# Optimization experiments

Hardware: AMD Instinct MI355X
Metric: run time of the kernel (lower is better)

Reference implementation:

```python
import jax, jax.numpy as jnp
import numpy as np

DIM = 1024
NUM_HEADS = 8  # only used for the scale; heads are never actually split
SCALE = float((DIM // NUM_HEADS) ** 0.5)


def _attn(x, wq, wk, wv):
    # Single-head full-dim attention, faithful to the source (no head split).
    Q = x @ wq.T  # [B,S,D]
    K = x @ wk.T
    V = x @ wv.T
    scores = jnp.einsum('bqd,bkd->bqk', Q, K) / SCALE  # [B,S,S]
    attn = jax.nn.softmax(scores, axis=-1)
    return jnp.einsum('bqk,bkd->bqd', attn, V)


def setup_inputs() -> dict:
    key = jax.random.key(0)
    ks = jax.random.split(key, 9)
    B, S, D = 4, 2048, DIM
    w = lambda k: jax.random.normal(k, (D, D), dtype=jnp.float32) * 0.02
    return {
        'x': jax.random.normal(ks[0], (B, S, D), dtype=jnp.float32),
        'wq1': w(ks[1]), 'wk1': w(ks[2]), 'wv1': w(ks[3]),
        'fc1_w': w(ks[4]),
        'wq2': w(ks[5]), 'wk2': w(ks[6]), 'wv2': w(ks[7]),
        'fc2_w': w(ks[8]),
    }


def reference(x, wq1, wk1, wv1, fc1_w, wq2, wk2, wv2, fc2_w):
    h = _attn(x, wq1, wk1, wv1)
    h = jax.nn.silu(h)
    h = h @ fc1_w.T
    h = _attn(h, wq2, wk2, wv2)
    h = jax.nn.silu(h)
    h = h @ fc2_w.T
    return jax.nn.softmax(h, axis=-1)
```

## Files before the change

kernel.cpp:

```cpp
#include <hip/hip_runtime.h>
#include <math.h>


typedef __attribute__((ext_vector_type(8))) int i32x8;
typedef __attribute__((ext_vector_type(4))) int i32x4;
typedef __attribute__((ext_vector_type(4))) float f32x4;
typedef unsigned char u8;
typedef unsigned int u32;

#define EPI_F32 0
#define EPI_F8 1
#define EPI_QKV 2
#define EPI_EXP 3
#define EPI_PV 4

__device__ __forceinline__ void gload_lds16(const void* g, void* l) {
    __builtin_amdgcn_global_load_lds(
        (const __attribute__((address_space(1))) void*)g,
        (__attribute__((address_space(3))) void*)l, 16, 0, 0);
}

__device__ __forceinline__ u8 cvt_f8(float v) {
    return (u8)(__builtin_amdgcn_cvt_pk_fp8_f32(v, v, 0, false) & 0xFF);
}

template <int EPI>
__global__ __launch_bounds__(256) void gemm_fp8(
    const u8* __restrict__ A, const u8* __restrict__ B,
    void* __restrict__ C0, void* __restrict__ C1, void* __restrict__ C2,
    int K, int ldA, int ldB, int ldC,
    long long bsA, long long bsB, long long bsC, float alpha, float beta)
{
    __shared__ u8 sA[128 * 128];
    __shared__ u8 sB[128 * 128];

    const int tid = threadIdx.x;
    const int wave = tid >> 6, lane = tid & 63;
    const int wm = wave >> 1, wn = wave & 1;
    const int m0 = blockIdx.y * 128, n0 = blockIdx.x * 128;
    const long long z = blockIdx.z;

    const u8* pA = A + z * bsA;
    const u8* pB = B + z * bsB;

    int blkid[4], rs_[4], cs16[4];
#pragma unroll
    for (int i = 0; i < 4; i++) {
        blkid[i] = wave * 256 + i * 64 + lane;
        rs_[i] = blkid[i] >> 3;
        cs16[i] = ((blkid[i] & 7) ^ (rs_[i] & 7)) * 16;
    }

    f32x4 acc[4][4] = {};
    const int fr = lane & 15, fc2 = (lane >> 4) * 2;

    for (int k0 = 0; k0 < K; k0 += 128) {
#pragma unroll
        for (int i = 0; i < 4; i++) {
            gload_lds16(pA + (long long)(m0 + rs_[i]) * ldA + k0 + cs16[i],
                        sA + blkid[i] * 16);
            gload_lds16(pB + (long long)(n0 + rs_[i]) * ldB + k0 + cs16[i],
                        sB + blkid[i] * 16);
        }
        __syncthreads();

        i32x8 a[4], b[4];
#pragma unroll
        for (int i = 0; i < 4; i++) {
            const int row = wm * 64 + i * 16 + fr;
            const int sw = row & 7;
            i32x4 lo = *(const i32x4*)(sA + row * 128 + ((fc2 + 0) ^ sw) * 16);
            i32x4 hi = *(const i32x4*)(sA + row * 128 + ((fc2 + 1) ^ sw) * 16);
            a[i] = __builtin_shufflevector(lo, hi, 0, 1, 2, 3, 4, 5, 6, 7);
        }
#pragma unroll
        for (int j = 0; j < 4; j++) {
            const int row = wn * 64 + j * 16 + fr;
            const int sw = row & 7;
            i32x4 lo = *(const i32x4*)(sB + row * 128 + ((fc2 + 0) ^ sw) * 16);
            i32x4 hi = *(const i32x4*)(sB + row * 128 + ((fc2 + 1) ^ sw) * 16);
            b[j] = __builtin_shufflevector(lo, hi, 0, 1, 2, 3, 4, 5, 6, 7);
        }
#pragma unroll
        for (int i = 0; i < 4; i++)
#pragma unroll
            for (int j = 0; j < 4; j++)
                acc[i][j] = __builtin_amdgcn_mfma_scale_f32_16x16x128_f8f6f4(
                    a[i], b[j], acc[i][j], 0 , 0 ,
                    0, 0x7F7F7F7F, 0, 0x7F7F7F7F);
        __syncthreads();
    }

    const int col = lane & 15;
    const int rbase = (lane >> 4) * 4;

    if (EPI == EPI_EXP) {
        u8* P = (u8*)C0 + z * bsC;
        float* rsum = (float*)C1 + z * 2048;
#pragma unroll
        for (int i = 0; i < 4; i++) {
            const int mloc = m0 + wm * 64 + i * 16 + rbase;
            float rowp[4] = {0.f, 0.f, 0.f, 0.f};
#pragma unroll
            for (int j = 0; j < 4; j++) {
                const int nloc = n0 + wn * 64 + j * 16 + col;
#pragma unroll
                for (int r = 0; r < 4; r++) {
                    float e = __expf(acc[i][j][r] * alpha);
                    rowp[r] += e;
                    P[(long long)(mloc + r) * ldC + nloc] = cvt_f8(e * 0.0625f);
                }
            }
#pragma unroll
            for (int r = 0; r < 4; r++) {
                float t = rowp[r];
                t += __shfl_xor(t, 1);
                t += __shfl_xor(t, 2);
                t += __shfl_xor(t, 4);
                t += __shfl_xor(t, 8);
                if ((lane & 15) == 0) atomicAdd(&rsum[mloc + r], t);
            }
        }
        return;
    }

#pragma unroll
    for (int i = 0; i < 4; i++) {
        const int mloc = m0 + wm * 64 + i * 16 + rbase;
        float inv[4];
        if (EPI == EPI_PV) {
            const float* rsum = (const float*)C1 + z * 2048;
#pragma unroll
            for (int r = 0; r < 4; r++) inv[r] = alpha / rsum[mloc + r];
        }
#pragma unroll
        for (int j = 0; j < 4; j++) {
            const int nloc = n0 + wn * 64 + j * 16 + col;
            if (EPI == EPI_F32) {
                float* C = (float*)C0 + z * bsC;
#pragma unroll
                for (int r = 0; r < 4; r++)
                    C[(long long)(mloc + r) * ldC + nloc] = acc[i][j][r] * alpha;
            } else if (EPI == EPI_F8) {
                u8* C = (u8*)C0 + z * bsC;
#pragma unroll
                for (int r = 0; r < 4; r++)
                    C[(long long)(mloc + r) * ldC + nloc] =
                        cvt_f8(acc[i][j][r] * alpha);
            } else if (EPI == EPI_PV) {
                u8* C = (u8*)C0 + z * bsC;
#pragma unroll
                for (int r = 0; r < 4; r++) {
                    float v = acc[i][j][r] * inv[r];
                    v = v / (1.f + __expf(-v));
                    C[(long long)(mloc + r) * ldC + nloc] = cvt_f8(v * beta);
                }
            } else {
                const int seg = nloc >> 10;
                const int nn = nloc & 1023;
                float v[4];
#pragma unroll
                for (int r = 0; r < 4; r++) v[r] = acc[i][j][r] * alpha;
                if (seg == 2) {
                    const int bb = mloc >> 11, mm = mloc & 2047;
                    int p01 = __builtin_amdgcn_cvt_pk_fp8_f32(v[0], v[1], 0, false);
                    int p23 = __builtin_amdgcn_cvt_pk_fp8_f32(v[2], v[3], 0, false);
                    u32 pk = (u32)(p01 & 0xFFFF) | ((u32)p23 << 16);
                    *(u32*)((u8*)C2 + (long long)bb * (1024LL * 2048) +
                            (long long)nn * 2048 + mm) = pk;
                } else {
                    u8* C = seg ? (u8*)C1 : (u8*)C0;
#pragma unroll
                    for (int r = 0; r < 4; r++)
                        C[(long long)(mloc + r) * 1024 + nn] = cvt_f8(v[r]);
                }
            }
        }
    }
}

__global__ __launch_bounds__(256) void convert_fp8(
    const float* __restrict__ in, u8* __restrict__ o, long long n, float scale)
{
    long long i = ((long long)blockIdx.x * 256 + threadIdx.x) * 4;
    if (i >= n) return;
    float4 v = *(const float4*)(in + i);
    int p01 = __builtin_amdgcn_cvt_pk_fp8_f32(v.x * scale, v.y * scale, 0, false);
    int p23 = __builtin_amdgcn_cvt_pk_fp8_f32(v.z * scale, v.w * scale, 0, false);
    *(u32*)(o + i) = (u32)(p01 & 0xFFFF) | ((u32)p23 << 16);
}

__global__ __launch_bounds__(256) void convert_w8(
    const float* w0, const float* w1, const float* w2, const float* w3,
    const float* w4, const float* w5, const float* w6, const float* w7,
    u8* __restrict__ o)
{
    const float* ws[8] = {w0, w1, w2, w3, w4, w5, w6, w7};
    const float* src = ws[blockIdx.y];
    long long i = ((long long)blockIdx.x * 256 + threadIdx.x) * 4;
    float4 v = *(const float4*)(src + i);
    int p01 = __builtin_amdgcn_cvt_pk_fp8_f32(v.x * 256.f, v.y * 256.f, 0, false);
    int p23 = __builtin_amdgcn_cvt_pk_fp8_f32(v.z * 256.f, v.w * 256.f, 0, false);
    *(u32*)(o + (long long)blockIdx.y * 1024 * 1024 + i) =
        (u32)(p01 & 0xFFFF) | ((u32)p23 << 16);
}

__global__ __launch_bounds__(256) void softmax_1024(
    const float* __restrict__ in, float* __restrict__ out)
{
    const float* p = in + (long long)blockIdx.x * 1024;
    float* o = out + (long long)blockIdx.x * 1024;
    const int tid = threadIdx.x;
    const int lane = tid & 63, wv = tid >> 6;
    __shared__ float redm[4], reds[4];

    float4 v = *(const float4*)(p + tid * 4);
    float vals[4] = {v.x, v.y, v.z, v.w};

    float m = -INFINITY;
#pragma unroll
    for (int i = 0; i < 4; i++) m = fmaxf(m, vals[i]);
#pragma unroll
    for (int off = 32; off; off >>= 1) m = fmaxf(m, __shfl_xor(m, off));
    if (lane == 0) redm[wv] = m;
    __syncthreads();
    m = fmaxf(fmaxf(redm[0], redm[1]), fmaxf(redm[2], redm[3]));

    float s = 0.f;
#pragma unroll
    for (int i = 0; i < 4; i++) {
        vals[i] = __expf(vals[i] - m);
        s += vals[i];
    }
#pragma unroll
    for (int off = 32; off; off >>= 1) s += __shfl_xor(s, off);
    if (lane == 0) reds[wv] = s;
    __syncthreads();
    s = reds[0] + reds[1] + reds[2] + reds[3];
    const float inv = 1.0f / s;
    float4 ov;
    ov.x = vals[0] * inv; ov.y = vals[1] * inv;
    ov.z = vals[2] * inv; ov.w = vals[3] * inv;
    *(float4*)(o + tid * 4) = ov;
}

extern "C" void kernel_launch(void* const* d_in, const int* in_sizes, int n_in,
                              void* d_out, int out_size, void* d_ws, size_t ws_size,
                              hipStream_t stream)
{
    const float* x = (const float*)d_in[0];
    float* out = (float*)d_out;

    constexpr int Bt = 4, S = 2048, D = 1024;
    constexpr int M = Bt * S;
    const long long MD = (long long)M * D;
    const long long DD = (long long)D * D;
    const long long SD = (long long)S * D;
    const long long SS = (long long)S * S;

    u8* Af = (u8*)d_ws;
    u8* Wf = Af + MD;
    u8* Qf = Wf + 8 * DD;
    u8* Kf = Qf + MD;
    u8* VT = Kf + MD;
    u8* Pf = VT + MD;
    u8* Hs = Pf + (long long)Bt * SS;
    float* SC = (float*)(Hs + MD);
    float* rsum = SC + MD;

    const dim3 blk(256);

    const float SOFT = 0.08838834764831845f;
    const float a_qkv[2] = {8.f / 2048.f, 1024.f / 65536.f};
    const float a_qk[2]  = {SOFT / 64.f, SOFT / 1048576.f};
    const float a_pv[2]  = {2.0f, 1.f / 64.f};
    const float b_pv[2]  = {256.f, 65536.f};
    const float a_fc[2]  = {256.f / 65536.f, 1.f / 16777216.f};

    convert_fp8<<<dim3((int)(MD / 1024)), blk, 0, stream>>>(x, Af, MD, 8.f);
    convert_w8<<<dim3((int)(DD / 1024), 8), blk, 0, stream>>>(
        (const float*)d_in[1], (const float*)d_in[2], (const float*)d_in[3],
        (const float*)d_in[4], (const float*)d_in[5], (const float*)d_in[6],
        (const float*)d_in[7], (const float*)d_in[8], Wf);

    const dim3 gqkv(3 * D / 128, M / 128, 1);
    const dim3 gw(D / 128, M / 128, 1);
    const dim3 gqk(S / 128, S / 128, Bt);
    const dim3 gpv(D / 128, S / 128, Bt);

    for (int layer = 0; layer < 2; layer++) {
        const u8* wqkv = Wf + (long long)(layer * 4) * DD;
        const u8* fc   = Wf + (long long)(layer * 4 + 3) * DD;

        gemm_fp8<EPI_QKV><<<gqkv, blk, 0, stream>>>(
            Af, wqkv, Qf, Kf, VT, D, D, D, D, 0, 0, 0, a_qkv[layer], 0.f);
        hipMemsetAsync(rsum, 0, (size_t)M * sizeof(float), stream);
        gemm_fp8<EPI_EXP><<<gqk, blk, 0, stream>>>(
            Qf, Kf, Pf, rsum, nullptr, D, D, D, S, SD, SD, SS,
            a_qk[layer], 0.f);
        gemm_fp8<EPI_PV><<<gpv, blk, 0, stream>>>(
            Pf, VT, Hs, rsum, nullptr, S, S, S, D, SS, (long long)D * S, SD,
            a_pv[layer], b_pv[layer]);
        if (layer == 0) {
            gemm_fp8<EPI_F8><<<gw, blk, 0, stream>>>(
                Hs, fc, Af, nullptr, nullptr, D, D, D, D, 0, 0, 0,
                a_fc[0], 0.f);
        } else {
            gemm_fp8<EPI_F32><<<gw, blk, 0, stream>>>(
                Hs, fc, SC, nullptr, nullptr, D, D, D, D, 0, 0, 0,
                a_fc[1], 0.f);
        }
    }

    softmax_1024<<<dim3(M), blk, 0, stream>>>(SC, out);
}
```

Measured before the change: 347.8 us.

## Switch FP8 GEMM to 32x32x64 MFMA and fold rsum zeroing into weight conversion

The FP8 GEMM now uses the 32x32x64 scaled MFMA with a 2x2 accumulator tile per wave instead of 4x4 tiles of 16x16x128. The K step is split into two halves, and every epilogue is remapped to the 32x32 output layout, including the row-sum shuffle reduction, the transposed V store and the per-row inverse loads. This is meant to cut LDS fragment reads and MFMA issue count for the same work. Separately, the per-layer hipMemsetAsync of the row-sum buffer is dropped. Both layers' sums are instead zeroed inside the weight-conversion kernel, using two separate buffers, which saves two launches but needs workspace room for the second buffer.

```diff
diff --git a/kernel.cpp b/kernel.cpp
--- a/kernel.cpp
+++ b/kernel.cpp
@@ -4,7 +4,7 @@
 
 typedef __attribute__((ext_vector_type(8))) int i32x8;
 typedef __attribute__((ext_vector_type(4))) int i32x4;
-typedef __attribute__((ext_vector_type(4))) float f32x4;
+typedef __attribute__((ext_vector_type(16))) float f32x16;
 typedef unsigned char u8;
 typedef unsigned int u32;
 
@@ -51,8 +51,10 @@
         cs16[i] = ((blkid[i] & 7) ^ (rs_[i] & 7)) * 16;
     }
 
-    f32x4 acc[4][4] = {};
-    const int fr = lane & 15, fc2 = (lane >> 4) * 2;
+    f32x16 acc[2][2] = {};
+    const int l31 = lane & 31;
+    const int lh = lane >> 5;
+    const int half4 = lh * 4;
 
     for (int k0 = 0; k0 < K; k0 += 128) {
 #pragma unroll
@@ -64,115 +66,138 @@
         }
         __syncthreads();
 
-        i32x8 a[4], b[4];
-#pragma unroll
-        for (int i = 0; i < 4; i++) {
-            const int row = wm * 64 + i * 16 + fr;
-            const int sw = row & 7;
-            i32x4 lo = *(const i32x4*)(sA + row * 128 + ((fc2 + 0) ^ sw) * 16);
-            i32x4 hi = *(const i32x4*)(sA + row * 128 + ((fc2 + 1) ^ sw) * 16);
-            a[i] = __builtin_shufflevector(lo, hi, 0, 1, 2, 3, 4, 5, 6, 7);
-        }
-#pragma unroll
-        for (int j = 0; j < 4; j++) {
-            const int row = wn * 64 + j * 16 + fr;
-            const int sw = row & 7;
-            i32x4 lo = *(const i32x4*)(sB + row * 128 + ((fc2 + 0) ^ sw) * 16);
-            i32x4 hi = *(const i32x4*)(sB + row * 128 + ((fc2 + 1) ^ sw) * 16);
-            b[j] = __builtin_shufflevector(lo, hi, 0, 1, 2, 3, 4, 5, 6, 7);
-        }
-#pragma unroll
-        for (int i = 0; i < 4; i++)
-#pragma unroll
-            for (int j = 0; j < 4; j++)
-                acc[i][j] = __builtin_amdgcn_mfma_scale_f32_16x16x128_f8f6f4(
-                    a[i], b[j], acc[i][j], 0 , 0 ,
-                    0, 0x7F7F7F7F, 0, 0x7F7F7F7F);
+#pragma unroll
+        for (int h = 0; h < 2; h++) {
+            const int c0 = h * 4 + lh * 2;
+            i32x8 a[2], b[2];
+#pragma unroll
+            for (int i = 0; i < 2; i++) {
+                const int row = wm * 64 + i * 32 + l31;
+                const int sw = row & 7;
+                i32x4 lo = *(const i32x4*)(sA + row * 128 + ((c0 + 0) ^ sw) * 16);
+                i32x4 hi = *(const i32x4*)(sA + row * 128 + ((c0 + 1) ^ sw) * 16);
+                a[i] = __builtin_shufflevector(lo, hi, 0, 1, 2, 3, 4, 5, 6, 7);
+            }
+#pragma unroll
+            for (int j = 0; j < 2; j++) {
+                const int row = wn * 64 + j * 32 + l31;
+                const int sw = row & 7;
+                i32x4 lo = *(const i32x4*)(sB + row * 128 + ((c0 + 0) ^ sw) * 16);
+                i32x4 hi = *(const i32x4*)(sB + row * 128 + ((c0 + 1) ^ sw) * 16);
+                b[j] = __builtin_shufflevector(lo, hi, 0, 1, 2, 3, 4, 5, 6, 7);
+            }
+#pragma unroll
+            for (int i = 0; i < 2; i++)
+#pragma unroll
+                for (int j = 0; j < 2; j++)
+                    acc[i][j] = __builtin_amdgcn_mfma_scale_f32_32x32x64_f8f6f4(
+                        a[i], b[j], acc[i][j], 0 , 0 ,
+                        0, 0x7F7F7F7F, 0, 0x7F7F7F7F);
+        }
         __syncthreads();
     }
 
-    const int col = lane & 15;
-    const int rbase = (lane >> 4) * 4;
+    const int col = l31;
 
     if (EPI == EPI_EXP) {
         u8* P = (u8*)C0 + z * bsC;
         float* rsum = (float*)C1 + z * 2048;
 #pragma unroll
-        for (int i = 0; i < 4; i++) {
-            const int mloc = m0 + wm * 64 + i * 16 + rbase;
-            float rowp[4] = {0.f, 0.f, 0.f, 0.f};
-#pragma unroll
-            for (int j = 0; j < 4; j++) {
-                const int nloc = n0 + wn * 64 + j * 16 + col;
-#pragma unroll
-                for (int r = 0; r < 4; r++) {
-                    float e = __expf(acc[i][j][r] * alpha);
-                    rowp[r] += e;
-                    P[(long long)(mloc + r) * ldC + nloc] = cvt_f8(e * 0.0625f);
-                }
-            }
-#pragma unroll
-            for (int r = 0; r < 4; r++) {
-                float t = rowp[r];
+        for (int i = 0; i < 2; i++) {
+            const int mbase = m0 + wm * 64 + i * 32;
+            float rowp[16];
+#pragma unroll
+            for (int g = 0; g < 16; g++) rowp[g] = 0.f;
+#pragma unroll
+            for (int j = 0; j < 2; j++) {
+                const int nloc = n0 + wn * 64 + j * 32 + col;
+#pragma unroll
+                for (int g = 0; g < 16; g++) {
+                    const int mloc = mbase + (g & 3) + 8 * (g >> 2) + half4;
+                    float e = __expf(acc[i][j][g] * alpha);
+                    rowp[g] += e;
+                    P[(long long)mloc * ldC + nloc] = cvt_f8(e * 0.0625f);
+                }
+            }
+#pragma unroll
+            for (int g = 0; g < 16; g++) {
+                float t = rowp[g];
                 t += __shfl_xor(t, 1);
                 t += __shfl_xor(t, 2);
                 t += __shfl_xor(t, 4);
                 t += __shfl_xor(t, 8);
-                if ((lane & 15) == 0) atomicAdd(&rsum[mloc + r], t);
+                t += __shfl_xor(t, 16);
+                if (col == 0) {
+                    const int mloc = mbase + (g & 3) + 8 * (g >> 2) + half4;
+                    atomicAdd(&rsum[mloc], t);
+                }
             }
         }
         return;
     }
 
 #pragma unroll
-    for (int i = 0; i < 4; i++) {
-        const int mloc = m0 + wm * 64 + i * 16 + rbase;
-        float inv[4];
+    for (int i = 0; i < 2; i++) {
+        const int mbase = m0 + wm * 64 + i * 32;
+        float inv[16];
         if (EPI == EPI_PV) {
             const float* rsum = (const float*)C1 + z * 2048;
 #pragma unroll
-            for (int r = 0; r < 4; r++) inv[r] = alpha / rsum[mloc + r];
-        }
-#pragma unroll
-        for (int j = 0; j < 4; j++) {
-            const int nloc = n0 + wn * 64 + j * 16 + col;
+            for (int g = 0; g < 16; g++)
+                inv[g] = alpha / rsum[mbase + (g & 3) + 8 * (g >> 2) + half4];
+        }
+#pragma unroll
+        for (int j = 0; j < 2; j++) {
+            const int nloc = n0 + wn * 64 + j * 32 + col;
             if (EPI == EPI_F32) {
                 float* C = (float*)C0 + z * bsC;
 #pragma unroll
-                for (int r = 0; r < 4; r++)
-                    C[(long long)(mloc + r) * ldC + nloc] = acc[i][j][r] * alpha;
+                for (int g = 0; g < 16; g++) {
+                    const int mloc = mbase + (g & 3) + 8 * (g >> 2) + half4;
+                    C[(long long)mloc * ldC + nloc] = acc[i][j][g] * alpha;
+                }
             } else if (EPI == EPI_F8) {
                 u8* C = (u8*)C0 + z * bsC;
 #pragma unroll
-                for (int r = 0; r < 4; r++)
-                    C[(long long)(mloc + r) * ldC + nloc] =
-                        cvt_f8(acc[i][j][r] * alpha);
+                for (int g = 0; g < 16; g++) {
+                    const int mloc = mbase + (g & 3) + 8 * (g >> 2) + half4;
+                    C[(long long)mloc * ldC + nloc] = cvt_f8(acc[i][j][g] * alpha);
+                }
             } else if (EPI == EPI_PV) {
                 u8* C = (u8*)C0 + z * bsC;
 #pragma unroll
-                for (int r = 0; r < 4; r++) {
-                    float v = acc[i][j][r] * inv[r];
+                for (int g = 0; g < 16; g++) {
+                    const int mloc = mbase + (g & 3) + 8 * (g >> 2) + half4;
+                    float v = acc[i][j][g] * inv[g];
                     v = v / (1.f + __expf(-v));
-                    C[(long long)(mloc + r) * ldC + nloc] = cvt_f8(v * beta);
+                    C[(long long)mloc * ldC + nloc] = cvt_f8(v * beta);
                 }
             } else {
                 const int seg = nloc >> 10;
                 const int nn = nloc & 1023;
-                float v[4];
-#pragma unroll
-                for (int r = 0; r < 4; r++) v[r] = acc[i][j][r] * alpha;
                 if (seg == 2) {
-                    const int bb = mloc >> 11, mm = mloc & 2047;
-                    int p01 = __builtin_amdgcn_cvt_pk_fp8_f32(v[0], v[1], 0, false);
-                    int p23 = __builtin_amdgcn_cvt_pk_fp8_f32(v[2], v[3], 0, false);
-                    u32 pk = (u32)(p01 & 0xFFFF) | ((u32)p23 << 16);
-                    *(u32*)((u8*)C2 + (long long)bb * (1024LL * 2048) +
-                            (long long)nn * 2048 + mm) = pk;
+#pragma unroll
+                    for (int g = 0; g < 4; g++) {
+                        const int mloc = mbase + 8 * g + half4;
+                        const int bb = mloc >> 11, mm = mloc & 2047;
+                        float v0 = acc[i][j][4 * g + 0] * alpha;
+                        float v1 = acc[i][j][4 * g + 1] * alpha;
+                        float v2 = acc[i][j][4 * g + 2] * alpha;
+                        float v3 = acc[i][j][4 * g + 3] * alpha;
+                        int p01 = __builtin_amdgcn_cvt_pk_fp8_f32(v0, v1, 0, false);
+                        int p23 = __builtin_amdgcn_cvt_pk_fp8_f32(v2, v3, 0, false);
+                        u32 pk = (u32)(p01 & 0xFFFF) | ((u32)p23 << 16);
+                        *(u32*)((u8*)C2 + (long long)bb * (1024LL * 2048) +
+                                (long long)nn * 2048 + mm) = pk;
+                    }
                 } else {
                     u8* C = seg ? (u8*)C1 : (u8*)C0;
 #pragma unroll
-                    for (int r = 0; r < 4; r++)
-                        C[(long long)(mloc + r) * 1024 + nn] = cvt_f8(v[r]);
+                    for (int g = 0; g < 16; g++) {
+                        const int mloc = mbase + (g & 3) + 8 * (g >> 2) + half4;
+                        C[(long long)mloc * 1024 + nn] =
+                            cvt_f8(acc[i][j][g] * alpha);
+                    }
                 }
             }
         }
@@ -193,8 +218,12 @@
 __global__ __launch_bounds__(256) void convert_w8(
     const float* w0, const float* w1, const float* w2, const float* w3,
     const float* w4, const float* w5, const float* w6, const float* w7,
-    u8* __restrict__ o)
-{
+    u8* __restrict__ o, float* __restrict__ rz)
+{
+    if (blockIdx.y == 0 && blockIdx.x < 16) {
+        float4 zero = {0.f, 0.f, 0.f, 0.f};
+        *(float4*)(rz + ((long long)blockIdx.x * 256 + threadIdx.x) * 4) = zero;
+    }
     const float* ws[8] = {w0, w1, w2, w3, w4, w5, w6, w7};
     const float* src = ws[blockIdx.y];
     long long i = ((long long)blockIdx.x * 256 + threadIdx.x) * 4;
@@ -266,7 +295,8 @@
     u8* Pf = VT + MD;
     u8* Hs = Pf + (long long)Bt * SS;
     float* SC = (float*)(Hs + MD);
-    float* rsum = SC + MD;
+    float* rsum0 = SC + MD;
+    float* rsum1 = rsum0 + M;
 
     const dim3 blk(256);
 
@@ -281,7 +311,7 @@
     convert_w8<<<dim3((int)(DD / 1024), 8), blk, 0, stream>>>(
         (const float*)d_in[1], (const float*)d_in[2], (const float*)d_in[3],
         (const float*)d_in[4], (const float*)d_in[5], (const float*)d_in[6],
-        (const float*)d_in[7], (const float*)d_in[8], Wf);
+        (const float*)d_in[7], (const float*)d_in[8], Wf, rsum0);
 
     const dim3 gqkv(3 * D / 128, M / 128, 1);
     const dim3 gw(D / 128, M / 128, 1);
@@ -291,10 +321,10 @@
     for (int layer = 0; layer < 2; layer++) {
         const u8* wqkv = Wf + (long long)(layer * 4) * DD;
         const u8* fc   = Wf + (long long)(layer * 4 + 3) * DD;
+        float* rsum    = layer ? rsum1 : rsum0;
 
         gemm_fp8<EPI_QKV><<<gqkv, blk, 0, stream>>>(
             Af, wqkv, Qf, Kf, VT, D, D, D, D, 0, 0, 0, a_qkv[layer], 0.f);
-        hipMemsetAsync(rsum, 0, (size_t)M * sizeof(float), stream);
         gemm_fp8<EPI_EXP><<<gqk, blk, 0, stream>>>(
             Qf, Kf, Pf, rsum, nullptr, D, D, D, S, SD, SD, SS,
             a_qk[layer], 0.f);
```

Result: slower. 373.4 us (+7.3%).

## Fuse final exp and row-sum into fc2 GEMM epilogue, merge conversions and memsets

Applied to the files above, without the earlier changes.

The last GEMM's epilogue now writes exp(logits) and atomically accumulates per-row sums, so the final softmax becomes a single normalize pass without max or sum reductions. The two input-conversion kernels are merged into one launch that also zeroes three row-sum buffers, which removes the per-layer memsets. This drops the max subtraction, so it relies on the logits staying small enough not to overflow, and it adds atomic traffic to the fc2 epilogue.

```diff
diff --git a/kernel.cpp b/kernel.cpp
--- a/kernel.cpp
+++ b/kernel.cpp
@@ -8,11 +8,11 @@
 typedef unsigned char u8;
 typedef unsigned int u32;
 
-#define EPI_F32 0
 #define EPI_F8 1
 #define EPI_QKV 2
 #define EPI_EXP 3
 #define EPI_PV 4
+#define EPI_EXPF32 5
 
 __device__ __forceinline__ void gload_lds16(const void* g, void* l) {
     __builtin_amdgcn_global_load_lds(
@@ -94,12 +94,13 @@
     const int col = lane & 15;
     const int rbase = (lane >> 4) * 4;
 
-    if (EPI == EPI_EXP) {
+    if (EPI == EPI_EXP || EPI == EPI_EXPF32) {
         u8* P = (u8*)C0 + z * bsC;
-        float* rsum = (float*)C1 + z * 2048;
+        float* Cw = (float*)C0 + z * bsC;
+        float* rsum = (EPI == EPI_EXP) ? ((float*)C1 + z * 2048) : (float*)C1;
 #pragma unroll
         for (int i = 0; i < 4; i++) {
-            const int mloc = m0 + wm * 64 + i * 16 + rbase;
+            const int mloc0 = m0 + wm * 64 + i * 16 + rbase;
             float rowp[4] = {0.f, 0.f, 0.f, 0.f};
 #pragma unroll
             for (int j = 0; j < 4; j++) {
@@ -108,7 +109,11 @@
                 for (int r = 0; r < 4; r++) {
                     float e = __expf(acc[i][j][r] * alpha);
                     rowp[r] += e;
-                    P[(long long)(mloc + r) * ldC + nloc] = cvt_f8(e * 0.0625f);
+                    if (EPI == EPI_EXP)
+                        P[(long long)(mloc0 + r) * ldC + nloc] =
+                            cvt_f8(e * 0.0625f);
+                    else
+                        Cw[(long long)(mloc0 + r) * ldC + nloc] = e;
                 }
             }
 #pragma unroll
@@ -118,7 +123,7 @@
                 t += __shfl_xor(t, 2);
                 t += __shfl_xor(t, 4);
                 t += __shfl_xor(t, 8);
-                if ((lane & 15) == 0) atomicAdd(&rsum[mloc + r], t);
+                if ((lane & 15) == 0) atomicAdd(&rsum[mloc0 + r], t);
             }
         }
         return;
@@ -126,26 +131,21 @@
 
 #pragma unroll
     for (int i = 0; i < 4; i++) {
-        const int mloc = m0 + wm * 64 + i * 16 + rbase;
+        const int mloc0 = m0 + wm * 64 + i * 16 + rbase;
         float inv[4];
         if (EPI == EPI_PV) {
             const float* rsum = (const float*)C1 + z * 2048;
 #pragma unroll
-            for (int r = 0; r < 4; r++) inv[r] = alpha / rsum[mloc + r];
+            for (int r = 0; r < 4; r++) inv[r] = alpha / rsum[mloc0 + r];
         }
 #pragma unroll
         for (int j = 0; j < 4; j++) {
             const int nloc = n0 + wn * 64 + j * 16 + col;
-            if (EPI == EPI_F32) {
-                float* C = (float*)C0 + z * bsC;
+            if (EPI == EPI_F8) {
+                u8* C = (u8*)C0 + z * bsC;
 #pragma unroll
                 for (int r = 0; r < 4; r++)
-                    C[(long long)(mloc + r) * ldC + nloc] = acc[i][j][r] * alpha;
-            } else if (EPI == EPI_F8) {
-                u8* C = (u8*)C0 + z * bsC;
-#pragma unroll
-                for (int r = 0; r < 4; r++)
-                    C[(long long)(mloc + r) * ldC + nloc] =
+                    C[(long long)(mloc0 + r) * ldC + nloc] =
                         cvt_f8(acc[i][j][r] * alpha);
             } else if (EPI == EPI_PV) {
                 u8* C = (u8*)C0 + z * bsC;
@@ -153,7 +153,7 @@
                 for (int r = 0; r < 4; r++) {
                     float v = acc[i][j][r] * inv[r];
                     v = v / (1.f + __expf(-v));
-                    C[(long long)(mloc + r) * ldC + nloc] = cvt_f8(v * beta);
+                    C[(long long)(mloc0 + r) * ldC + nloc] = cvt_f8(v * beta);
                 }
             } else {
                 const int seg = nloc >> 10;
@@ -162,7 +162,7 @@
 #pragma unroll
                 for (int r = 0; r < 4; r++) v[r] = acc[i][j][r] * alpha;
                 if (seg == 2) {
-                    const int bb = mloc >> 11, mm = mloc & 2047;
+                    const int bb = mloc0 >> 11, mm = mloc0 & 2047;
                     int p01 = __builtin_amdgcn_cvt_pk_fp8_f32(v[0], v[1], 0, false);
                     int p23 = __builtin_amdgcn_cvt_pk_fp8_f32(v[2], v[3], 0, false);
                     u32 pk = (u32)(p01 & 0xFFFF) | ((u32)p23 << 16);
@@ -172,83 +172,62 @@
                     u8* C = seg ? (u8*)C1 : (u8*)C0;
 #pragma unroll
                     for (int r = 0; r < 4; r++)
-                        C[(long long)(mloc + r) * 1024 + nn] = cvt_f8(v[r]);
+                        C[(long long)(mloc0 + r) * 1024 + nn] = cvt_f8(v[r]);
                 }
             }
         }
     }
 }
 
-__global__ __launch_bounds__(256) void convert_fp8(
-    const float* __restrict__ in, u8* __restrict__ o, long long n, float scale)
-{
-    long long i = ((long long)blockIdx.x * 256 + threadIdx.x) * 4;
-    if (i >= n) return;
-    float4 v = *(const float4*)(in + i);
+__global__ __launch_bounds__(256) void convert_all(
+    const float* x, const float* w0, const float* w1, const float* w2,
+    const float* w3, const float* w4, const float* w5, const float* w6,
+    const float* w7, u8* __restrict__ ax, u8* __restrict__ wf,
+    float* __restrict__ rz)
+{
+    const int bid = blockIdx.x;
+    if (bid < 24) {
+        float4 zero = {0.f, 0.f, 0.f, 0.f};
+        *(float4*)(rz + ((long long)bid * 256 + threadIdx.x) * 4) = zero;
+    }
+    const float* src;
+    u8* dst;
+    float scale;
+    long long i;
+    if (bid < 8192) {
+        src = x; dst = ax; scale = 8.f;
+        i = ((long long)bid * 256 + threadIdx.x) * 4;
+    } else {
+        const float* ws[8] = {w0, w1, w2, w3, w4, w5, w6, w7};
+        const int wi = (bid - 8192) >> 10;
+        src = ws[wi]; scale = 256.f;
+        dst = wf + (long long)wi * 1024 * 1024;
+        i = (((long long)(bid - 8192) & 1023) * 256 + threadIdx.x) * 4;
+    }
+    float4 v = *(const float4*)(src + i);
     int p01 = __builtin_amdgcn_cvt_pk_fp8_f32(v.x * scale, v.y * scale, 0, false);
     int p23 = __builtin_amdgcn_cvt_pk_fp8_f32(v.z * scale, v.w * scale, 0, false);
-    *(u32*)(o + i) = (u32)(p01 & 0xFFFF) | ((u32)p23 << 16);
-}
-
-__global__ __launch_bounds__(256) void convert_w8(
-    const float* w0, const float* w1, const float* w2, const float* w3,
-    const float* w4, const float* w5, const float* w6, const float* w7,
-    u8* __restrict__ o)
-{
-    const float* ws[8] = {w0, w1, w2, w3, w4, w5, w6, w7};
-    const float* src = ws[blockIdx.y];
-    long long i = ((long long)blockIdx.x * 256 + threadIdx.x) * 4;
-    float4 v = *(const float4*)(src + i);
-    int p01 = __builtin_amdgcn_cvt_pk_fp8_f32(v.x * 256.f, v.y * 256.f, 0, false);
-    int p23 = __builtin_amdgcn_cvt_pk_fp8_f32(v.z * 256.f, v.w * 256.f, 0, false);
-    *(u32*)(o + (long long)blockIdx.y * 1024 * 1024 + i) =
-        (u32)(p01 & 0xFFFF) | ((u32)p23 << 16);
-}
-
-__global__ __launch_bounds__(256) void softmax_1024(
-    const float* __restrict__ in, float* __restrict__ out)
-{
-    const float* p = in + (long long)blockIdx.x * 1024;
-    float* o = out + (long long)blockIdx.x * 1024;
-    const int tid = threadIdx.x;
-    const int lane = tid & 63, wv = tid >> 6;
-    __shared__ float redm[4], reds[4];
-
-    float4 v = *(const float4*)(p + tid * 4);
-    float vals[4] = {v.x, v.y, v.z, v.w};
-
-    float m = -INFINITY;
-#pragma unroll
-    for (int i = 0; i < 4; i++) m = fmaxf(m, vals[i]);
-#pragma unroll
-    for (int off = 32; off; off >>= 1) m = fmaxf(m, __shfl_xor(m, off));
-    if (lane == 0) redm[wv] = m;
-    __syncthreads();
-    m = fmaxf(fmaxf(redm[0], redm[1]), fmaxf(redm[2], redm[3]));
-
-    float s = 0.f;
-#pragma unroll
-    for (int i = 0; i < 4; i++) {
-        vals[i] = __expf(vals[i] - m);
-        s += vals[i];
-    }
-#pragma unroll
-    for (int off = 32; off; off >>= 1) s += __shfl_xor(s, off);
-    if (lane == 0) reds[wv] = s;
-    __syncthreads();
-    s = reds[0] + reds[1] + reds[2] + reds[3];
-    const float inv = 1.0f / s;
+    *(u32*)(dst + i) = (u32)(p01 & 0xFFFF) | ((u32)p23 << 16);
+}
+
+__global__ __launch_bounds__(256) void normalize_1024(
+    const float* __restrict__ e, const float* __restrict__ rsum,
+    float* __restrict__ out)
+{
+    const long long row = blockIdx.x;
+    const float inv = 1.0f / rsum[row];
+    const float* p = e + row * 1024;
+    float* o = out + row * 1024;
+    float4 v = *(const float4*)(p + threadIdx.x * 4);
     float4 ov;
-    ov.x = vals[0] * inv; ov.y = vals[1] * inv;
-    ov.z = vals[2] * inv; ov.w = vals[3] * inv;
-    *(float4*)(o + tid * 4) = ov;
+    ov.x = v.x * inv; ov.y = v.y * inv; ov.z = v.z * inv; ov.w = v.w * inv;
+    *(float4*)(o + threadIdx.x * 4) = ov;
 }
 
 extern "C" void kernel_launch(void* const* d_in, const int* in_sizes, int n_in,
                               void* d_out, int out_size, void* d_ws, size_t ws_size,
                               hipStream_t stream)
 {
-    const float* x = (const float*)d_in[0];
     float* out = (float*)d_out;
 
     constexpr int Bt = 4, S = 2048, D = 1024;
@@ -266,7 +245,9 @@
     u8* Pf = VT + MD;
     u8* Hs = Pf + (long long)Bt * SS;
     float* SC = (float*)(Hs + MD);
-    float* rsum = SC + MD;
+    float* rsum0 = SC + MD;
+    float* rsum1 = rsum0 + M;
+    float* rsum2 = rsum1 + M;
 
     const dim3 blk(256);
 
@@ -277,11 +258,11 @@
     const float b_pv[2]  = {256.f, 65536.f};
     const float a_fc[2]  = {256.f / 65536.f, 1.f / 16777216.f};
 
-    convert_fp8<<<dim3((int)(MD / 1024)), blk, 0, stream>>>(x, Af, MD, 8.f);
-    convert_w8<<<dim3((int)(DD / 1024), 8), blk, 0, stream>>>(
-        (const float*)d_in[1], (const float*)d_in[2], (const float*)d_in[3],
-        (const float*)d_in[4], (const float*)d_in[5], (const float*)d_in[6],
-        (const float*)d_in[7], (const float*)d_in[8], Wf);
+    convert_all<<<dim3(16384), blk, 0, stream>>>(
+        (const float*)d_in[0], (const float*)d_in[1], (const float*)d_in[2],
+        (const float*)d_in[3], (const float*)d_in[4], (const float*)d_in[5],
+        (const float*)d_in[6], (const float*)d_in[7], (const float*)d_in[8],
+        Af, Wf, rsum0);
 
     const dim3 gqkv(3 * D / 128, M / 128, 1);
     const dim3 gw(D / 128, M / 128, 1);
@@ -291,10 +272,10 @@
     for (int layer = 0; layer < 2; layer++) {
         const u8* wqkv = Wf + (long long)(layer * 4) * DD;
         const u8* fc   = Wf + (long long)(layer * 4 + 3) * DD;
+        float* rsum    = layer ? rsum1 : rsum0;
 
         gemm_fp8<EPI_QKV><<<gqkv, blk, 0, stream>>>(
             Af, wqkv, Qf, Kf, VT, D, D, D, D, 0, 0, 0, a_qkv[layer], 0.f);
-        hipMemsetAsync(rsum, 0, (size_t)M * sizeof(float), stream);
         gemm_fp8<EPI_EXP><<<gqk, blk, 0, stream>>>(
             Qf, Kf, Pf, rsum, nullptr, D, D, D, S, SD, SD, SS,
             a_qk[layer], 0.f);
@@ -306,11 +287,11 @@
                 Hs, fc, Af, nullptr, nullptr, D, D, D, D, 0, 0, 0,
                 a_fc[0], 0.f);
         } else {
-            gemm_fp8<EPI_F32><<<gw, blk, 0, stream>>>(
-                Hs, fc, SC, nullptr, nullptr, D, D, D, D, 0, 0, 0,
+            gemm_fp8<EPI_EXPF32><<<gw, blk, 0, stream>>>(
+                Hs, fc, SC, rsum2, nullptr, D, D, D, D, 0, 0, 0,
                 a_fc[1], 0.f);
         }
     }
 
-    softmax_1024<<<dim3(M), blk, 0, stream>>>(SC, out);
-}
+    normalize_1024<<<dim3(M), blk, 0, stream>>>(SC, rsum2, out);
+}
```

Result: no change. 352.8 us (+1.4%).
